# Kernel tuning notes

Hardware: AMD Instinct MI355X
Metric: run time of the kernel (lower is better)

The kernel has to match this reference:

```python
import jax, jax.numpy as jnp
import numpy as np

# (multiplicity, irrep_dim) for irreps_in == irreps_out: 128x0e + 64x1o + 32x2e
IRREPS = [(128, 1), (64, 3), (32, 5)]
NUM_INDICES = 64
N_ELEMENTS = 8192
SCALE = 1.0  # module's `scale` arg; total coeff = scale / sqrt(num_indices) / sqrt(mul_in)
W_DIM = sum(m * m for m, _ in IRREPS)  # 21504


def setup_inputs() -> dict:
    key = jax.random.key(0)
    ks = jax.random.split(key, 5)
    x0 = jax.random.normal(ks[0], (N_ELEMENTS, 128, 1), jnp.float32)
    x1 = jax.random.normal(ks[1], (N_ELEMENTS, 64, 3), jnp.float32)
    x2 = jax.random.normal(ks[2], (N_ELEMENTS, 32, 5), jnp.float32)
    w = jax.random.normal(ks[3], (NUM_INDICES, W_DIM), jnp.float32)
    # Random contiguous segment sizes that sum exactly to N_ELEMENTS:
    bnd = jnp.sort(jax.random.randint(ks[4], (NUM_INDICES - 1,), 0, N_ELEMENTS + 1)).astype(jnp.int32)
    counts = jnp.diff(jnp.concatenate([jnp.zeros((1,), jnp.int32), bnd,
                                       jnp.full((1,), N_ELEMENTS, jnp.int32)]))
    return {"x0": x0, "x1": x1, "x2": x2, "w": w, "num_index_counts": counts}


def reference(x0, x1, x2, w, num_index_counts):
    """Indexed (segmented) equivariant linear: rows are grouped contiguously by
    num_index_counts; segment g uses weight row w[g]. Per matched irrep the
    weight block is a (mul_in, mul_out) mixing matrix applied identically to
    each of the ir.dim components (Schur's lemma), with fan-in normalization
    1/sqrt(mul_in) (cue.descriptors.linear) times scale/sqrt(num_indices)."""
    n = x0.shape[0]
    # segment id per row (rows are already grouped contiguously, as in Repeats())
    sid = jnp.repeat(jnp.arange(NUM_INDICES), num_index_counts, total_repeat_length=n)
    xs = (x0, x1, x2)
    ys = []
    off = 0
    for xk, (mul, ir_dim) in zip(xs, IRREPS):
        blk = w[:, off:off + mul * mul].reshape(NUM_INDICES, mul, mul)  # (E, m_in, m_out)
        coeff = float(SCALE / np.sqrt(NUM_INDICES) / np.sqrt(mul))
        wk = blk[sid]  # (n, m_in, m_out) per-row weight gather
        # y[n, o, i] = coeff * sum_m x[n, m, i] * w[g(n), m, o]
        ys.append(coeff * jnp.einsum('nmi,nmo->noi', xk, wk))
        off += mul * mul
    return tuple(ys)
```

## Files before the change

kernel.cpp:

```cpp
#include <hip/hip_runtime.h>

typedef __attribute__((ext_vector_type(8))) short bf16x8;
typedef __attribute__((ext_vector_type(4))) float f32x4;

#define NSEG 64
#define NROW 8192
#define WROW 21504
#define NBPP 576
#define T0   64
#define T12  16
#define PA   136
#define P1   196
#define P2   164

__device__ __forceinline__ unsigned short f2bf(float f) {
    unsigned u = __float_as_uint(f);
    u += 0x7fffu + ((u >> 16) & 1u);
    return (unsigned short)(u >> 16);
}

__global__ __launch_bounds__(256) void prep_kernel(
    const float* __restrict__ x0, const float* __restrict__ w,
    unsigned short* __restrict__ x0b, unsigned short* __restrict__ wt)
{
    const int t = threadIdx.x;
    const int b = blockIdx.x;
    if (b < 1024) {
        int i = b * 256 + t;
        float4 v = ((const float4*)x0)[i];
        ushort4 o;
        o.x = f2bf(v.x); o.y = f2bf(v.y); o.z = f2bf(v.z); o.w = f2bf(v.w);
        *(ushort4*)(x0b + (size_t)i * 4) = o;
    } else {
        __shared__ float lw[128 * 132];
        const int g = b - 1024;
        const float* wseg = w + (size_t)g * WROW;
        #pragma unroll
        for (int i = 0; i < 16; ++i) {
            int idx = t + i * 256;
            int r = idx >> 5, c4 = (idx & 31) * 4;
            float4 v = *(const float4*)(wseg + (size_t)r * 128 + c4);
            *(float4*)(lw + r * 132 + c4) = v;
        }
        __syncthreads();
        unsigned short* wo = wt + (size_t)g * 16384;
        #pragma unroll
        for (int i = 0; i < 16; ++i) {
            int idx = t + i * 256;
            int o = idx >> 5, k0 = (idx & 31) * 4;
            ushort4 v;
            v.x = f2bf(lw[(k0 + 0) * 132 + o]);
            v.y = f2bf(lw[(k0 + 1) * 132 + o]);
            v.z = f2bf(lw[(k0 + 2) * 132 + o]);
            v.w = f2bf(lw[(k0 + 3) * 132 + o]);
            *(ushort4*)(wo + (size_t)o * 128 + k0) = v;
        }
    }
}

__global__ __launch_bounds__(256) void iil_kernel(
    const float* __restrict__ x1, const float* __restrict__ x2,
    const float* __restrict__ w, const int* __restrict__ counts,
    const unsigned short* __restrict__ x0b, const unsigned short* __restrict__ wt,
    float* __restrict__ y0, float* __restrict__ y1, float* __restrict__ y2)
{
    __shared__ __align__(16) unsigned short smem_u[T0 * PA];
    __shared__ int sstart[NSEG + 1];
    __shared__ int t16s[NSEG + 1];
    __shared__ int t64s[NSEG + 1];

    const int t = threadIdx.x;

    if (t < NSEG) {
        int c = counts[t];
        int v = c;
        #pragma unroll
        for (int d = 1; d < NSEG; d <<= 1) {
            int u = __shfl_up(v, d, 64);
            if (t >= d) v += u;
        }
        sstart[t + 1] = v;
        int a = (c + 15) >> 4;
        #pragma unroll
        for (int d = 1; d < NSEG; d <<= 1) {
            int u = __shfl_up(a, d, 64);
            if (t >= d) a += u;
        }
        t16s[t + 1] = a;
        int b2 = (c + 63) >> 6;
        #pragma unroll
        for (int d = 1; d < NSEG; d <<= 1) {
            int u = __shfl_up(b2, d, 64);
            if (t >= d) b2 += u;
        }
        t64s[t + 1] = b2;
        if (t == 0) { sstart[0] = 0; t16s[0] = 0; t64s[0] = 0; }
    }
    __syncthreads();

    const int phase = blockIdx.x / NBPP;
    const int pb = blockIdx.x - phase * NBPP;
    const float4 z4 = make_float4(0.f, 0.f, 0.f, 0.f);
    float* sbuf = (float*)smem_u;

    if (phase == 0) {
        if (pb >= t64s[NSEG]) return;
        int lo = 0, hi = NSEG;
        while (hi - lo > 1) {
            int mid = (lo + hi) >> 1;
            if (t64s[mid] <= pb) lo = mid; else hi = mid;
        }
        const int g = lo;
        const int s = sstart[g] + (pb - t64s[g]) * T0;
        const int nr = min(T0, sstart[g + 1] - s);

        unsigned short* As = smem_u;
        {
            const uint4* src = (const uint4*)(x0b + (size_t)s * 128);
            const uint4 zz = make_uint4(0u, 0u, 0u, 0u);
            #pragma unroll
            for (int i = 0; i < 4; ++i) {
                int idx = t + i * 256;
                int r = idx >> 4, c8 = idx & 15;
                uint4 v = (r < nr) ? src[idx] : zz;
                *(uint4*)(As + r * PA + c8 * 8) = v;
            }
        }
        __syncthreads();

        const int lane = t & 63;
        const int wv = t >> 6;
        const int l16 = lane & 15;
        const int quad = lane >> 4;
        const int mp = wv & 1;
        const int np = wv >> 1;

        f32x4 acc[2][4];
        #pragma unroll
        for (int mt = 0; mt < 2; ++mt)
            #pragma unroll
            for (int nt = 0; nt < 4; ++nt)
                acc[mt][nt] = (f32x4){0.f, 0.f, 0.f, 0.f};

        const unsigned short* Abase = As + ((2 * mp) * 16 + l16) * PA + quad * 8;
        const unsigned short* Bbase = wt + (size_t)g * 16384
                                    + (size_t)((4 * np) * 16 + l16) * 128 + quad * 8;

        #pragma unroll
        for (int ks = 0; ks < 4; ++ks) {
            const int ko = ks * 32;
            bf16x8 a0 = *(const bf16x8*)(Abase + ko);
            bf16x8 a1 = *(const bf16x8*)(Abase + 16 * PA + ko);
            #pragma unroll
            for (int nt = 0; nt < 4; ++nt) {
                bf16x8 bfr = *(const bf16x8*)(Bbase + (size_t)nt * 16 * 128 + ko);
                acc[0][nt] = __builtin_amdgcn_mfma_f32_16x16x32_bf16(a0, bfr, acc[0][nt], 0, 0, 0);
                acc[1][nt] = __builtin_amdgcn_mfma_f32_16x16x32_bf16(a1, bfr, acc[1][nt], 0, 0, 0);
            }
        }

        const float c0 = 0.011048543456039806f;
        #pragma unroll
        for (int mt = 0; mt < 2; ++mt) {
            int rbase = (2 * mp + mt) * 16 + quad * 4;
            #pragma unroll
            for (int nt = 0; nt < 4; ++nt) {
                int col = (4 * np + nt) * 16 + l16;
                #pragma unroll
                for (int rg = 0; rg < 4; ++rg) {
                    int r = rbase + rg;
                    if (r < nr)
                        y0[(size_t)(s + r) * 128 + col] = acc[mt][nt][rg] * c0;
                }
            }
        }
    } else if (phase == 1) {
        if (pb >= t16s[NSEG]) return;
        int lo = 0, hi = NSEG;
        while (hi - lo > 1) {
            int mid = (lo + hi) >> 1;
            if (t16s[mid] <= pb) lo = mid; else hi = mid;
        }
        const int g = lo;
        const int s = sstart[g] + (pb - t16s[g]) * T12;
        const int nr = min(T12, sstart[g + 1] - s);
        const float* __restrict__ wseg = w + (size_t)g * WROW;

        float* sx1 = sbuf;
        const float4* g1 = (const float4*)x1 + (size_t)s * 48;
        #pragma unroll
        for (int i = 0; i < 3; ++i) {
            int idx = t + i * 256;
            int r = idx / 48, c = idx - r * 48;
            float4 v = (r < nr) ? g1[idx] : z4;
            *(float4*)(sx1 + r * P1 + c * 4) = v;
        }
        __syncthreads();

        const int og = t & 15;
        const int r = t >> 4;
        const float* xrow = sx1 + r * P1;
        const float* wp = wseg + 16384 + og * 4;
        float acc[12];
        #pragma unroll
        for (int i = 0; i < 12; ++i) acc[i] = 0.f;
        #pragma unroll 2
        for (int kq = 0; kq < 16; ++kq) {
            float4 xq0 = *(const float4*)(xrow + 12 * kq + 0);
            float4 xq1 = *(const float4*)(xrow + 12 * kq + 4);
            float4 xq2 = *(const float4*)(xrow + 12 * kq + 8);
            float xf[12] = {xq0.x, xq0.y, xq0.z, xq0.w,
                            xq1.x, xq1.y, xq1.z, xq1.w,
                            xq2.x, xq2.y, xq2.z, xq2.w};
            #pragma unroll
            for (int kk = 0; kk < 4; ++kk) {
                float4 wv = *(const float4*)(wp + (size_t)(4 * kq + kk) * 64);
                #pragma unroll
                for (int oo = 0; oo < 4; ++oo) {
                    float wvo = (oo == 0) ? wv.x : (oo == 1) ? wv.y : (oo == 2) ? wv.z : wv.w;
                    acc[oo * 3 + 0] = fmaf(wvo, xf[kk * 3 + 0], acc[oo * 3 + 0]);
                    acc[oo * 3 + 1] = fmaf(wvo, xf[kk * 3 + 1], acc[oo * 3 + 1]);
                    acc[oo * 3 + 2] = fmaf(wvo, xf[kk * 3 + 2], acc[oo * 3 + 2]);
                }
            }
        }
        const float c1 = 0.015625f;
        if (r < nr) {
            float* yb = y1 + (size_t)(s + r) * 192 + og * 12;
            *(float4*)(yb + 0) = make_float4(acc[0] * c1, acc[1] * c1, acc[2] * c1, acc[3] * c1);
            *(float4*)(yb + 4) = make_float4(acc[4] * c1, acc[5] * c1, acc[6] * c1, acc[7] * c1);
            *(float4*)(yb + 8) = make_float4(acc[8] * c1, acc[9] * c1, acc[10] * c1, acc[11] * c1);
        }
    } else {
        if (pb >= t16s[NSEG]) return;
        int lo = 0, hi = NSEG;
        while (hi - lo > 1) {
            int mid = (lo + hi) >> 1;
            if (t16s[mid] <= pb) lo = mid; else hi = mid;
        }
        const int g = lo;
        const int s = sstart[g] + (pb - t16s[g]) * T12;
        const int nr = min(T12, sstart[g + 1] - s);
        const float* __restrict__ wseg = w + (size_t)g * WROW;

        float* sx2 = sbuf;
        const float4* g2 = (const float4*)x2 + (size_t)s * 40;
        #pragma unroll
        for (int i = 0; i < 3; ++i) {
            int idx = t + i * 256;
            if (idx < 640) {
                int r = idx / 40, c = idx - r * 40;
                float4 v = (r < nr) ? g2[idx] : z4;
                *(float4*)(sx2 + r * P2 + c * 4) = v;
            }
        }
        __syncthreads();

        const int og = t & 15;
        const int r = t >> 4;
        const float* xrow = sx2 + r * P2;
        const float* wp = wseg + 20480 + og * 2;
        float acc[10];
        #pragma unroll
        for (int i = 0; i < 10; ++i) acc[i] = 0.f;
        #pragma unroll
        for (int kq = 0; kq < 8; ++kq) {
            float xf[20];
            #pragma unroll
            for (int j = 0; j < 5; ++j) {
                float4 v = *(const float4*)(xrow + 20 * kq + 4 * j);
                xf[4 * j + 0] = v.x; xf[4 * j + 1] = v.y; xf[4 * j + 2] = v.z; xf[4 * j + 3] = v.w;
            }
            #pragma unroll
            for (int kk = 0; kk < 4; ++kk) {
                float2 wv = *(const float2*)(wp + (size_t)(4 * kq + kk) * 32);
                #pragma unroll
                for (int i = 0; i < 5; ++i) {
                    acc[i]     = fmaf(wv.x, xf[5 * kk + i], acc[i]);
                    acc[5 + i] = fmaf(wv.y, xf[5 * kk + i], acc[5 + i]);
                }
            }
        }
        const float c2 = 0.022097086912079608f;
        if (r < nr) {
            float* yb = y2 + (size_t)(s + r) * 160 + og * 10;
            #pragma unroll
            for (int i = 0; i < 5; ++i)
                *(float2*)(yb + 2 * i) = make_float2(acc[2 * i] * c2, acc[2 * i + 1] * c2);
        }
    }
}

extern "C" void kernel_launch(void* const* d_in, const int* in_sizes, int n_in,
                              void* d_out, int out_size, void* d_ws, size_t ws_size,
                              hipStream_t stream) {
    const float* x0 = (const float*)d_in[0];
    const float* x1 = (const float*)d_in[1];
    const float* x2 = (const float*)d_in[2];
    const float* w  = (const float*)d_in[3];
    const int* counts = (const int*)d_in[4];

    float* y0 = (float*)d_out;
    float* y1 = y0 + (size_t)NROW * 128;
    float* y2 = y1 + (size_t)NROW * 192;

    unsigned short* x0b = (unsigned short*)d_ws;
    unsigned short* wtp = x0b + (size_t)NROW * 128;

    hipLaunchKernelGGL(prep_kernel, dim3(1024 + NSEG), dim3(256), 0, stream,
                       x0, w, x0b, wtp);
    hipLaunchKernelGGL(iil_kernel, dim3(3 * NBPP), dim3(256), 0, stream,
                       x1, x2, w, counts, x0b, wtp, y0, y1, y2);
}
```

Baseline: 99.05 us.

## Move l=1 and l=2 irrep paths to bf16 MFMA with transposed prep

The prep kernel now also converts x1 and x2 to bf16 in a component-major layout (rows = node×component, cols = multiplicity) and transposes the w1 and w2 weight blocks to bf16. The main kernel replaces the scalar FMA loops for the 1o and 2e irreps with 16x16x32 bf16 MFMA tiles. It uses a uniform 32-row tile for all three phases (x0 tiles shrink from 64 rows), cutting the grid from 3×576 to 3×320 blocks. This targets ALU-bound scalar work, at the cost of an extra prep pass over x1/x2, extra workspace traffic, bf16 rounding on those paths, and strided scalar output stores.

```diff
diff --git a/kernel.cpp b/kernel.cpp
--- a/kernel.cpp
+++ b/kernel.cpp
@@ -6,12 +6,10 @@
 #define NSEG 64
 #define NROW 8192
 #define WROW 21504
-#define NBPP 576
-#define T0   64
-#define T12  16
-#define PA   136
-#define P1   196
-#define P2   164
+#define NBPP 320
+#define PA0  136
+#define PA1  72
+#define PA2  40
 
 __device__ __forceinline__ unsigned short f2bf(float f) {
     unsigned u = __float_as_uint(f);
@@ -20,8 +18,12 @@
 }
 
 __global__ __launch_bounds__(256) void prep_kernel(
-    const float* __restrict__ x0, const float* __restrict__ w,
-    unsigned short* __restrict__ x0b, unsigned short* __restrict__ wt)
+    const float* __restrict__ x0, const float* __restrict__ x1, const float* __restrict__ x2,
+    const float* __restrict__ w,
+    unsigned short* __restrict__ x0b, unsigned short* __restrict__ x1b,
+    unsigned short* __restrict__ x2b,
+    unsigned short* __restrict__ w0t, unsigned short* __restrict__ w1t,
+    unsigned short* __restrict__ w2t)
 {
     const int t = threadIdx.x;
     const int b = blockIdx.x;
@@ -31,9 +33,33 @@
         ushort4 o;
         o.x = f2bf(v.x); o.y = f2bf(v.y); o.z = f2bf(v.z); o.w = f2bf(v.w);
         *(ushort4*)(x0b + (size_t)i * 4) = o;
+    } else if (b < 2048) {
+        if (t < 192) {
+            int n = (b - 1024) * 8 + (t / 24);
+            int j = t % 24;
+            int i = j >> 3, m0 = (j & 7) * 8;
+            const float* src = x1 + (size_t)n * 192;
+            unsigned short us[8];
+            #pragma unroll
+            for (int u = 0; u < 8; ++u)
+                us[u] = f2bf(src[(m0 + u) * 3 + i]);
+            *(uint4*)(x1b + (size_t)n * 192 + j * 8) = *(uint4*)us;
+        }
+    } else if (b < 3072) {
+        if (t < 160) {
+            int n = (b - 2048) * 8 + (t / 20);
+            int j = t % 20;
+            int i = j >> 2, m0 = (j & 3) * 8;
+            const float* src = x2 + (size_t)n * 160;
+            unsigned short us[8];
+            #pragma unroll
+            for (int u = 0; u < 8; ++u)
+                us[u] = f2bf(src[(m0 + u) * 5 + i]);
+            *(uint4*)(x2b + (size_t)n * 160 + j * 8) = *(uint4*)us;
+        }
     } else {
         __shared__ float lw[128 * 132];
-        const int g = b - 1024;
+        const int g = b - 3072;
         const float* wseg = w + (size_t)g * WROW;
         #pragma unroll
         for (int i = 0; i < 16; ++i) {
@@ -43,31 +69,80 @@
             *(float4*)(lw + r * 132 + c4) = v;
         }
         __syncthreads();
-        unsigned short* wo = wt + (size_t)g * 16384;
-        #pragma unroll
-        for (int i = 0; i < 16; ++i) {
-            int idx = t + i * 256;
-            int o = idx >> 5, k0 = (idx & 31) * 4;
+        {
+            unsigned short* wo = w0t + (size_t)g * 16384;
+            #pragma unroll
+            for (int i = 0; i < 16; ++i) {
+                int idx = t + i * 256;
+                int o = idx >> 5, k0 = (idx & 31) * 4;
+                ushort4 v;
+                v.x = f2bf(lw[(k0 + 0) * 132 + o]);
+                v.y = f2bf(lw[(k0 + 1) * 132 + o]);
+                v.z = f2bf(lw[(k0 + 2) * 132 + o]);
+                v.w = f2bf(lw[(k0 + 3) * 132 + o]);
+                *(ushort4*)(wo + (size_t)o * 128 + k0) = v;
+            }
+        }
+        __syncthreads();
+        {
+            const float* w1 = wseg + 16384;
+            #pragma unroll
+            for (int i = 0; i < 4; ++i) {
+                int idx = t + i * 256;
+                int m = idx >> 4, o4 = (idx & 15) * 4;
+                float4 v = *(const float4*)(w1 + (size_t)m * 64 + o4);
+                *(float4*)(lw + m * 68 + o4) = v;
+            }
+        }
+        __syncthreads();
+        {
+            unsigned short* wo = w1t + (size_t)g * 4096;
+            #pragma unroll
+            for (int i = 0; i < 4; ++i) {
+                int idx = t + i * 256;
+                int o = idx >> 4, m0 = (idx & 15) * 4;
+                ushort4 v;
+                v.x = f2bf(lw[(m0 + 0) * 68 + o]);
+                v.y = f2bf(lw[(m0 + 1) * 68 + o]);
+                v.z = f2bf(lw[(m0 + 2) * 68 + o]);
+                v.w = f2bf(lw[(m0 + 3) * 68 + o]);
+                *(ushort4*)(wo + (size_t)o * 64 + m0) = v;
+            }
+        }
+        __syncthreads();
+        {
+            const float* w2 = wseg + 20480;
+            int idx = t;
+            int m = idx >> 3, o4 = (idx & 7) * 4;
+            float4 v = *(const float4*)(w2 + (size_t)m * 32 + o4);
+            *(float4*)(lw + m * 36 + o4) = v;
+        }
+        __syncthreads();
+        {
+            unsigned short* wo = w2t + (size_t)g * 1024;
+            int idx = t;
+            int o = idx >> 3, m0 = (idx & 7) * 4;
             ushort4 v;
-            v.x = f2bf(lw[(k0 + 0) * 132 + o]);
-            v.y = f2bf(lw[(k0 + 1) * 132 + o]);
-            v.z = f2bf(lw[(k0 + 2) * 132 + o]);
-            v.w = f2bf(lw[(k0 + 3) * 132 + o]);
-            *(ushort4*)(wo + (size_t)o * 128 + k0) = v;
+            v.x = f2bf(lw[(m0 + 0) * 36 + o]);
+            v.y = f2bf(lw[(m0 + 1) * 36 + o]);
+            v.z = f2bf(lw[(m0 + 2) * 36 + o]);
+            v.w = f2bf(lw[(m0 + 3) * 36 + o]);
+            *(ushort4*)(wo + (size_t)o * 32 + m0) = v;
         }
     }
 }
 
 __global__ __launch_bounds__(256) void iil_kernel(
-    const float* __restrict__ x1, const float* __restrict__ x2,
-    const float* __restrict__ w, const int* __restrict__ counts,
-    const unsigned short* __restrict__ x0b, const unsigned short* __restrict__ wt,
+    const int* __restrict__ counts,
+    const unsigned short* __restrict__ x0b, const unsigned short* __restrict__ x1b,
+    const unsigned short* __restrict__ x2b,
+    const unsigned short* __restrict__ w0t, const unsigned short* __restrict__ w1t,
+    const unsigned short* __restrict__ w2t,
     float* __restrict__ y0, float* __restrict__ y1, float* __restrict__ y2)
 {
-    __shared__ __align__(16) unsigned short smem_u[T0 * PA];
+    __shared__ __align__(16) unsigned short As[96 * PA1];
     __shared__ int sstart[NSEG + 1];
-    __shared__ int t16s[NSEG + 1];
-    __shared__ int t64s[NSEG + 1];
+    __shared__ int t32s[NSEG + 1];
 
     const int t = threadIdx.x;
 
@@ -80,213 +155,164 @@
             if (t >= d) v += u;
         }
         sstart[t + 1] = v;
-        int a = (c + 15) >> 4;
+        int a = (c + 31) >> 5;
         #pragma unroll
         for (int d = 1; d < NSEG; d <<= 1) {
             int u = __shfl_up(a, d, 64);
             if (t >= d) a += u;
         }
-        t16s[t + 1] = a;
-        int b2 = (c + 63) >> 6;
-        #pragma unroll
-        for (int d = 1; d < NSEG; d <<= 1) {
-            int u = __shfl_up(b2, d, 64);
-            if (t >= d) b2 += u;
-        }
-        t64s[t + 1] = b2;
-        if (t == 0) { sstart[0] = 0; t16s[0] = 0; t64s[0] = 0; }
+        t32s[t + 1] = a;
+        if (t == 0) { sstart[0] = 0; t32s[0] = 0; }
     }
     __syncthreads();
 
     const int phase = blockIdx.x / NBPP;
     const int pb = blockIdx.x - phase * NBPP;
-    const float4 z4 = make_float4(0.f, 0.f, 0.f, 0.f);
-    float* sbuf = (float*)smem_u;
+    if (pb >= t32s[NSEG]) return;
+
+    int lo = 0, hi = NSEG;
+    while (hi - lo > 1) {
+        int mid = (lo + hi) >> 1;
+        if (t32s[mid] <= pb) lo = mid; else hi = mid;
+    }
+    const int g = lo;
+    const int s = sstart[g] + (pb - t32s[g]) * 32;
+    const int nr = min(32, sstart[g + 1] - s);
+
+    const int lane = t & 63;
+    const int wv = t >> 6;
+    const int l16 = lane & 15;
+    const int quad = lane >> 4;
+    const uint4 zz = make_uint4(0u, 0u, 0u, 0u);
 
     if (phase == 0) {
-        if (pb >= t64s[NSEG]) return;
-        int lo = 0, hi = NSEG;
-        while (hi - lo > 1) {
-            int mid = (lo + hi) >> 1;
-            if (t64s[mid] <= pb) lo = mid; else hi = mid;
-        }
-        const int g = lo;
-        const int s = sstart[g] + (pb - t64s[g]) * T0;
-        const int nr = min(T0, sstart[g + 1] - s);
-
-        unsigned short* As = smem_u;
         {
             const uint4* src = (const uint4*)(x0b + (size_t)s * 128);
-            const uint4 zz = make_uint4(0u, 0u, 0u, 0u);
-            #pragma unroll
-            for (int i = 0; i < 4; ++i) {
+            #pragma unroll
+            for (int i = 0; i < 2; ++i) {
                 int idx = t + i * 256;
                 int r = idx >> 4, c8 = idx & 15;
                 uint4 v = (r < nr) ? src[idx] : zz;
-                *(uint4*)(As + r * PA + c8 * 8) = v;
-            }
-        }
-        __syncthreads();
-
-        const int lane = t & 63;
-        const int wv = t >> 6;
-        const int l16 = lane & 15;
-        const int quad = lane >> 4;
-        const int mp = wv & 1;
+                *(uint4*)(As + r * PA0 + c8 * 8) = v;
+            }
+        }
+        __syncthreads();
+
+        const int mt = wv & 1;
         const int np = wv >> 1;
-
-        f32x4 acc[2][4];
-        #pragma unroll
-        for (int mt = 0; mt < 2; ++mt)
-            #pragma unroll
-            for (int nt = 0; nt < 4; ++nt)
-                acc[mt][nt] = (f32x4){0.f, 0.f, 0.f, 0.f};
-
-        const unsigned short* Abase = As + ((2 * mp) * 16 + l16) * PA + quad * 8;
-        const unsigned short* Bbase = wt + (size_t)g * 16384
-                                    + (size_t)((4 * np) * 16 + l16) * 128 + quad * 8;
-
+        f32x4 acc[4];
+        #pragma unroll
+        for (int nt = 0; nt < 4; ++nt) acc[nt] = (f32x4){0.f, 0.f, 0.f, 0.f};
+
+        const unsigned short* Ab = As + (mt * 16 + l16) * PA0 + quad * 8;
+        const unsigned short* Bb = w0t + (size_t)g * 16384
+                                 + (size_t)((np * 4) * 16 + l16) * 128 + quad * 8;
         #pragma unroll
         for (int ks = 0; ks < 4; ++ks) {
-            const int ko = ks * 32;
-            bf16x8 a0 = *(const bf16x8*)(Abase + ko);
-            bf16x8 a1 = *(const bf16x8*)(Abase + 16 * PA + ko);
+            bf16x8 a = *(const bf16x8*)(Ab + ks * 32);
             #pragma unroll
             for (int nt = 0; nt < 4; ++nt) {
-                bf16x8 bfr = *(const bf16x8*)(Bbase + (size_t)nt * 16 * 128 + ko);
-                acc[0][nt] = __builtin_amdgcn_mfma_f32_16x16x32_bf16(a0, bfr, acc[0][nt], 0, 0, 0);
-                acc[1][nt] = __builtin_amdgcn_mfma_f32_16x16x32_bf16(a1, bfr, acc[1][nt], 0, 0, 0);
-            }
-        }
-
+                bf16x8 bf = *(const bf16x8*)(Bb + (size_t)nt * 2048 + ks * 32);
+                acc[nt] = __builtin_amdgcn_mfma_f32_16x16x32_bf16(a, bf, acc[nt], 0, 0, 0);
+            }
+        }
         const float c0 = 0.011048543456039806f;
-        #pragma unroll
-        for (int mt = 0; mt < 2; ++mt) {
-            int rbase = (2 * mp + mt) * 16 + quad * 4;
-            #pragma unroll
-            for (int nt = 0; nt < 4; ++nt) {
-                int col = (4 * np + nt) * 16 + l16;
-                #pragma unroll
-                for (int rg = 0; rg < 4; ++rg) {
-                    int r = rbase + rg;
-                    if (r < nr)
-                        y0[(size_t)(s + r) * 128 + col] = acc[mt][nt][rg] * c0;
+        const int rbase = mt * 16 + quad * 4;
+        #pragma unroll
+        for (int nt = 0; nt < 4; ++nt) {
+            int col = (np * 4 + nt) * 16 + l16;
+            #pragma unroll
+            for (int rg = 0; rg < 4; ++rg) {
+                int r = rbase + rg;
+                if (r < nr)
+                    y0[(size_t)(s + r) * 128 + col] = acc[nt][rg] * c0;
+            }
+        }
+    } else if (phase == 1) {
+        {
+            const uint4* src = (const uint4*)(x1b + (size_t)s * 192);
+            #pragma unroll
+            for (int i = 0; i < 3; ++i) {
+                int idx = t + i * 256;
+                int nl = idx / 24, j = idx % 24;
+                int ii = j >> 3, m0 = (j & 7) * 8;
+                uint4 v = (nl < nr) ? src[idx] : zz;
+                *(uint4*)(As + (nl * 3 + ii) * PA1 + m0) = v;
+            }
+        }
+        __syncthreads();
+
+        const int nt = wv;
+        f32x4 acc[6];
+        #pragma unroll
+        for (int mt = 0; mt < 6; ++mt) acc[mt] = (f32x4){0.f, 0.f, 0.f, 0.f};
+
+        const unsigned short* Bb = w1t + (size_t)g * 4096
+                                 + (size_t)(nt * 16 + l16) * 64 + quad * 8;
+        bf16x8 b0 = *(const bf16x8*)(Bb);
+        bf16x8 b1 = *(const bf16x8*)(Bb + 32);
+        #pragma unroll
+        for (int mt = 0; mt < 6; ++mt) {
+            const unsigned short* Ab = As + (mt * 16 + l16) * PA1 + quad * 8;
+            bf16x8 a0 = *(const bf16x8*)(Ab);
+            bf16x8 a1 = *(const bf16x8*)(Ab + 32);
+            acc[mt] = __builtin_amdgcn_mfma_f32_16x16x32_bf16(a0, b0, acc[mt], 0, 0, 0);
+            acc[mt] = __builtin_amdgcn_mfma_f32_16x16x32_bf16(a1, b1, acc[mt], 0, 0, 0);
+        }
+        const float c1 = 0.015625f;
+        const int col = nt * 16 + l16;
+        #pragma unroll
+        for (int mt = 0; mt < 6; ++mt) {
+            #pragma unroll
+            for (int rg = 0; rg < 4; ++rg) {
+                int R = mt * 16 + quad * 4 + rg;
+                int nl = R / 3, ii = R - nl * 3;
+                if (nl < nr)
+                    y1[(size_t)(s + nl) * 192 + col * 3 + ii] = acc[mt][rg] * c1;
+            }
+        }
+    } else {
+        {
+            const uint4* src = (const uint4*)(x2b + (size_t)s * 160);
+            #pragma unroll
+            for (int i = 0; i < 3; ++i) {
+                int idx = t + i * 256;
+                if (idx < 640) {
+                    int nl = idx / 20, j = idx % 20;
+                    int ii = j >> 2, m0 = (j & 3) * 8;
+                    uint4 v = (nl < nr) ? src[idx] : zz;
+                    *(uint4*)(As + (nl * 5 + ii) * PA2 + m0) = v;
                 }
             }
         }
-    } else if (phase == 1) {
-        if (pb >= t16s[NSEG]) return;
-        int lo = 0, hi = NSEG;
-        while (hi - lo > 1) {
-            int mid = (lo + hi) >> 1;
-            if (t16s[mid] <= pb) lo = mid; else hi = mid;
-        }
-        const int g = lo;
-        const int s = sstart[g] + (pb - t16s[g]) * T12;
-        const int nr = min(T12, sstart[g + 1] - s);
-        const float* __restrict__ wseg = w + (size_t)g * WROW;
-
-        float* sx1 = sbuf;
-        const float4* g1 = (const float4*)x1 + (size_t)s * 48;
-        #pragma unroll
-        for (int i = 0; i < 3; ++i) {
-            int idx = t + i * 256;
-            int r = idx / 48, c = idx - r * 48;
-            float4 v = (r < nr) ? g1[idx] : z4;
-            *(float4*)(sx1 + r * P1 + c * 4) = v;
-        }
-        __syncthreads();
-
-        const int og = t & 15;
-        const int r = t >> 4;
-        const float* xrow = sx1 + r * P1;
-        const float* wp = wseg + 16384 + og * 4;
-        float acc[12];
-        #pragma unroll
-        for (int i = 0; i < 12; ++i) acc[i] = 0.f;
-        #pragma unroll 2
-        for (int kq = 0; kq < 16; ++kq) {
-            float4 xq0 = *(const float4*)(xrow + 12 * kq + 0);
-            float4 xq1 = *(const float4*)(xrow + 12 * kq + 4);
-            float4 xq2 = *(const float4*)(xrow + 12 * kq + 8);
-            float xf[12] = {xq0.x, xq0.y, xq0.z, xq0.w,
-                            xq1.x, xq1.y, xq1.z, xq1.w,
-                            xq2.x, xq2.y, xq2.z, xq2.w};
-            #pragma unroll
-            for (int kk = 0; kk < 4; ++kk) {
-                float4 wv = *(const float4*)(wp + (size_t)(4 * kq + kk) * 64);
-                #pragma unroll
-                for (int oo = 0; oo < 4; ++oo) {
-                    float wvo = (oo == 0) ? wv.x : (oo == 1) ? wv.y : (oo == 2) ? wv.z : wv.w;
-                    acc[oo * 3 + 0] = fmaf(wvo, xf[kk * 3 + 0], acc[oo * 3 + 0]);
-                    acc[oo * 3 + 1] = fmaf(wvo, xf[kk * 3 + 1], acc[oo * 3 + 1]);
-                    acc[oo * 3 + 2] = fmaf(wvo, xf[kk * 3 + 2], acc[oo * 3 + 2]);
-                }
-            }
-        }
-        const float c1 = 0.015625f;
-        if (r < nr) {
-            float* yb = y1 + (size_t)(s + r) * 192 + og * 12;
-            *(float4*)(yb + 0) = make_float4(acc[0] * c1, acc[1] * c1, acc[2] * c1, acc[3] * c1);
-            *(float4*)(yb + 4) = make_float4(acc[4] * c1, acc[5] * c1, acc[6] * c1, acc[7] * c1);
-            *(float4*)(yb + 8) = make_float4(acc[8] * c1, acc[9] * c1, acc[10] * c1, acc[11] * c1);
-        }
-    } else {
-        if (pb >= t16s[NSEG]) return;
-        int lo = 0, hi = NSEG;
-        while (hi - lo > 1) {
-            int mid = (lo + hi) >> 1;
-            if (t16s[mid] <= pb) lo = mid; else hi = mid;
-        }
-        const int g = lo;
-        const int s = sstart[g] + (pb - t16s[g]) * T12;
-        const int nr = min(T12, sstart[g + 1] - s);
-        const float* __restrict__ wseg = w + (size_t)g * WROW;
-
-        float* sx2 = sbuf;
-        const float4* g2 = (const float4*)x2 + (size_t)s * 40;
-        #pragma unroll
-        for (int i = 0; i < 3; ++i) {
-            int idx = t + i * 256;
-            if (idx < 640) {
-                int r = idx / 40, c = idx - r * 40;
-                float4 v = (r < nr) ? g2[idx] : z4;
-                *(float4*)(sx2 + r * P2 + c * 4) = v;
-            }
-        }
-        __syncthreads();
-
-        const int og = t & 15;
-        const int r = t >> 4;
-        const float* xrow = sx2 + r * P2;
-        const float* wp = wseg + 20480 + og * 2;
-        float acc[10];
-        #pragma unroll
-        for (int i = 0; i < 10; ++i) acc[i] = 0.f;
-        #pragma unroll
-        for (int kq = 0; kq < 8; ++kq) {
-            float xf[20];
-            #pragma unroll
-            for (int j = 0; j < 5; ++j) {
-                float4 v = *(const float4*)(xrow + 20 * kq + 4 * j);
-                xf[4 * j + 0] = v.x; xf[4 * j + 1] = v.y; xf[4 * j + 2] = v.z; xf[4 * j + 3] = v.w;
-            }
-            #pragma unroll
-            for (int kk = 0; kk < 4; ++kk) {
-                float2 wv = *(const float2*)(wp + (size_t)(4 * kq + kk) * 32);
-                #pragma unroll
-                for (int i = 0; i < 5; ++i) {
-                    acc[i]     = fmaf(wv.x, xf[5 * kk + i], acc[i]);
-                    acc[5 + i] = fmaf(wv.y, xf[5 * kk + i], acc[5 + i]);
-                }
-            }
+        __syncthreads();
+
+        const int mh = wv & 1;
+        const int nt = wv >> 1;
+        f32x4 acc[5];
+        #pragma unroll
+        for (int mt = 0; mt < 5; ++mt) acc[mt] = (f32x4){0.f, 0.f, 0.f, 0.f};
+
+        const unsigned short* Bb = w2t + (size_t)g * 1024
+                                 + (size_t)(nt * 16 + l16) * 32 + quad * 8;
+        bf16x8 b0 = *(const bf16x8*)(Bb);
+        #pragma unroll
+        for (int mt = 0; mt < 5; ++mt) {
+            const unsigned short* Ab = As + ((mh * 5 + mt) * 16 + l16) * PA2 + quad * 8;
+            bf16x8 a0 = *(const bf16x8*)(Ab);
+            acc[mt] = __builtin_amdgcn_mfma_f32_16x16x32_bf16(a0, b0, acc[mt], 0, 0, 0);
         }
         const float c2 = 0.022097086912079608f;
-        if (r < nr) {
-            float* yb = y2 + (size_t)(s + r) * 160 + og * 10;
-            #pragma unroll
-            for (int i = 0; i < 5; ++i)
-                *(float2*)(yb + 2 * i) = make_float2(acc[2 * i] * c2, acc[2 * i + 1] * c2);
+        const int col = nt * 16 + l16;
+        #pragma unroll
+        for (int mt = 0; mt < 5; ++mt) {
+            #pragma unroll
+            for (int rg = 0; rg < 4; ++rg) {
+                int R = (mh * 5 + mt) * 16 + quad * 4 + rg;
+                int nl = R / 5, ii = R - nl * 5;
+                if (nl < nr)
+                    y2[(size_t)(s + nl) * 160 + col * 5 + ii] = acc[mt][rg] * c2;
+            }
         }
     }
 }
@@ -305,10 +331,14 @@
     float* y2 = y1 + (size_t)NROW * 192;
 
     unsigned short* x0b = (unsigned short*)d_ws;
-    unsigned short* wtp = x0b + (size_t)NROW * 128;
-
-    hipLaunchKernelGGL(prep_kernel, dim3(1024 + NSEG), dim3(256), 0, stream,
-                       x0, w, x0b, wtp);
+    unsigned short* x1b = x0b + (size_t)NROW * 128;
+    unsigned short* x2b = x1b + (size_t)NROW * 192;
+    unsigned short* w0t = x2b + (size_t)NROW * 160;
+    unsigned short* w1t = w0t + (size_t)NSEG * 16384;
+    unsigned short* w2t = w1t + (size_t)NSEG * 4096;
+
+    hipLaunchKernelGGL(prep_kernel, dim3(3072 + NSEG), dim3(256), 0, stream,
+                       x0, x1, x2, w, x0b, x1b, x2b, w0t, w1t, w2t);
     hipLaunchKernelGGL(iil_kernel, dim3(3 * NBPP), dim3(256), 0, stream,
-                       x1, x2, w, counts, x0b, wtp, y0, y1, y2);
+                       counts, x0b, x1b, x2b, w0t, w1t, w2t, y0, y1, y2);
 }
```

After: 98.53 us. Within noise of the previous version (-0.5%).
